# Kernel optimization log

Measured on AMD Instinct MI355X. Metric: run time of the kernel, lower is better.

## Reference

```python
import jax, jax.numpy as jnp
import numpy as np

B, S, D, H, E, TOP_K = 4, 2048, 1024, 2048, 8, 2


def setup_inputs() -> dict:
    key = jax.random.key(0)
    ks = jax.random.split(key, 5)
    scale_d = 1.0 / np.sqrt(D)
    scale_h = 1.0 / np.sqrt(H)
    return {
        "x": jax.random.normal(ks[0], (B, S, D), dtype=jnp.float32),
        "gate_w": jax.random.normal(ks[1], (D, E), dtype=jnp.float32) * scale_d,
        "w1": jax.random.normal(ks[2], (E, D, H), dtype=jnp.float32) * scale_d,
        "w2": jax.random.normal(ks[3], (E, D, H), dtype=jnp.float32) * scale_d,
        "w3": jax.random.normal(ks[4], (E, H, D), dtype=jnp.float32) * scale_h,
    }


def reference(x, gate_w, w1, w2, w3):
    # Gating: softmax over experts, keep top-k probs, renormalize.
    gate_scores = jax.nn.softmax(x @ gate_w, axis=-1)          # [B,S,E]
    top_vals, top_idx = jax.lax.top_k(gate_scores, TOP_K)      # [B,S,K]
    mask = (jax.nn.one_hot(top_idx, E, dtype=x.dtype) * top_vals[..., None]).sum(axis=-2)  # [B,S,E]
    weights = mask / (mask.sum(axis=-1, keepdims=True) + 1e-9)
    # Dense SwiGLU over ALL experts (faithful to the original ModuleList loop).
    g = jax.nn.silu(jnp.einsum('bsd,edh->bseh', x, w1)) * jnp.einsum('bsd,edh->bseh', x, w2)  # [B,S,E,H]
    expert_out = jnp.einsum('bseh,ehd->bsed', g, w3)           # [B,S,E,D]
    # Masked weighted combine (dropout is identity in eval / p=0).
    return jnp.einsum('bse,bsed->bsd', weights, expert_out)    # [B,S,D]
```

## Files before the change

kernel.cpp:

```cpp
#include <hip/hip_runtime.h>

#define T_TOK 8192
#define DDIM 1024
#define HDIM 2048
#define NEXP 8

typedef __attribute__((ext_vector_type(8))) short short8;
typedef __attribute__((ext_vector_type(4))) float f32x4;

#define WAITV8 asm volatile("s_waitcnt vmcnt(8)" ::: "memory")
#define WAITV0 asm volatile("s_waitcnt vmcnt(0)" ::: "memory")
#define WAITL0 asm volatile("s_waitcnt lgkmcnt(0)" ::: "memory")
#define SCHEDB __builtin_amdgcn_sched_barrier(0)
#define BARRIER __builtin_amdgcn_s_barrier()

__device__ __forceinline__ unsigned short f2bf(float f) {
  unsigned int u = __builtin_bit_cast(unsigned int, f);
  u += 0x7fffu + ((u >> 16) & 1u);
  return (unsigned short)(u >> 16);
}
__device__ __forceinline__ float bf2f(unsigned short h) {
  unsigned int u = ((unsigned int)h) << 16;
  return __builtin_bit_cast(float, u);
}
__device__ __forceinline__ void gload16(const void* g, void* l) {
  __builtin_amdgcn_global_load_lds((const __attribute__((address_space(1))) void*)g,
                                   (__attribute__((address_space(3))) void*)l, 16, 0, 0);
}
__device__ __forceinline__ int imin(int a, int b) { return a < b ? a : b; }

__global__ __launch_bounds__(256) void cvt_kernel(const float* __restrict__ in,
                                                  unsigned short* __restrict__ out, int n) {
  int i = (blockIdx.x * 256 + threadIdx.x) * 8;
  int stride = gridDim.x * 256 * 8;
  for (; i < n; i += stride) {
    float4 a = *(const float4*)(in + i);
    float4 b = *(const float4*)(in + i + 4);
    alignas(16) unsigned short t[8] = {f2bf(a.x), f2bf(a.y), f2bf(a.z), f2bf(a.w),
                                       f2bf(b.x), f2bf(b.y), f2bf(b.z), f2bf(b.w)};
    *(uint4*)(out + i) = *(const uint4*)t;
  }
}

__global__ __launch_bounds__(256) void tcvt_kernel(const float* __restrict__ in,
                                                   unsigned short* __restrict__ out,
                                                   int R, int C, size_t outEstride,
                                                   int perm, int s16) {
  int e = blockIdx.z;
  int rb = blockIdx.y * 64, cb = blockIdx.x * 64;
  const float* inE = in + (size_t)e * R * C;
  unsigned short* outE = out + (size_t)e * outEstride;
  __shared__ float tile[64][65];
  int tid = threadIdx.x;
  #pragma unroll
  for (int i = 0; i < 4; ++i) {
    int f = tid + i * 256;
    int r = f >> 4, c4 = (f & 15) << 2;
    float4 v = *(const float4*)(inE + (size_t)(rb + r) * C + cb + c4);
    tile[r][c4] = v.x; tile[r][c4 + 1] = v.y; tile[r][c4 + 2] = v.z; tile[r][c4 + 3] = v.w;
  }
  __syncthreads();
  #pragma unroll
  for (int i = 0; i < 2; ++i) {
    int g = tid + i * 256;
    int oc = g >> 3;
    int r8 = (g & 7) << 3;
    alignas(16) unsigned short tmp[8];
    #pragma unroll
    for (int j = 0; j < 8; ++j) tmp[j] = f2bf(tile[r8 + j][oc]);
    int orow = cb + oc;
    int orow2 = perm ? (32 * (orow >> 4) + (orow & 15) + s16) : orow;
    *(uint4*)(outE + (size_t)orow2 * R + rb + r8) = *(const uint4*)tmp;
  }
}

__global__ __launch_bounds__(256) void gate_kernel(const float* __restrict__ x,
                                                   const float* __restrict__ gw,
                                                   int* __restrict__ t_exp,
                                                   float* __restrict__ t_w) {
  int t = blockIdx.x * 4 + (threadIdx.x >> 6);
  int lane = threadIdx.x & 63;
  const float* xp = x + (size_t)t * DDIM;
  float acc[NEXP];
  #pragma unroll
  for (int e = 0; e < NEXP; ++e) acc[e] = 0.f;
  for (int i = 0; i < DDIM / 64; ++i) {
    int d = i * 64 + lane;
    float xv = xp[d];
    const float* g = gw + d * NEXP;
    #pragma unroll
    for (int e = 0; e < NEXP; ++e) acc[e] += xv * g[e];
  }
  #pragma unroll
  for (int off = 32; off > 0; off >>= 1) {
    #pragma unroll
    for (int e = 0; e < NEXP; ++e) acc[e] += __shfl_xor(acc[e], off, 64);
  }
  float mx = acc[0];
  #pragma unroll
  for (int e = 1; e < NEXP; ++e) mx = fmaxf(mx, acc[e]);
  float p[NEXP]; float S = 0.f;
  #pragma unroll
  for (int e = 0; e < NEXP; ++e) { p[e] = expf(acc[e] - mx); S += p[e]; }
  int i0 = 0; float v0 = p[0];
  #pragma unroll
  for (int e = 1; e < NEXP; ++e) if (p[e] > v0) { v0 = p[e]; i0 = e; }
  int i1 = -1; float v1 = -1.f;
  #pragma unroll
  for (int e = 0; e < NEXP; ++e) if (e != i0 && p[e] > v1) { v1 = p[e]; i1 = e; }
  float pv0 = v0 / S, pv1 = v1 / S;
  float denom = pv0 + pv1 + 1e-9f;
  if (lane == 0) {
    t_exp[t * 2] = i0; t_exp[t * 2 + 1] = i1;
    t_w[t * 2] = pv0 / denom; t_w[t * 2 + 1] = pv1 / denom;
  }
}

__global__ __launch_bounds__(1024) void partition_kernel(
    const int* __restrict__ t_exp, const float* __restrict__ t_w,
    int* __restrict__ ctrl, int* __restrict__ row_tok,
    float* __restrict__ row_w, int* __restrict__ inv_row) {
  int tid = threadIdx.x;
  int wv = tid >> 6, lane = tid & 63;
  __shared__ int wtot[16][8];
  __shared__ int wbase[16][8];
  __shared__ int soff[8];

  int t0 = tid * 8;
  int exps[16];
  int c[8];
  #pragma unroll
  for (int e = 0; e < 8; ++e) c[e] = 0;
  #pragma unroll
  for (int s = 0; s < 16; ++s) {
    exps[s] = t_exp[t0 * 2 + s];
    #pragma unroll
    for (int e = 0; e < 8; ++e) c[e] += (exps[s] == e);
  }
  int inc[8];
  #pragma unroll
  for (int e = 0; e < 8; ++e) inc[e] = c[e];
  #pragma unroll
  for (int d = 1; d < 64; d <<= 1) {
    #pragma unroll
    for (int e = 0; e < 8; ++e) {
      int v = __shfl_up(inc[e], d, 64);
      if (lane >= d) inc[e] += v;
    }
  }
  if (lane == 63) {
    #pragma unroll
    for (int e = 0; e < 8; ++e) wtot[wv][e] = inc[e];
  }
  __syncthreads();
  if (wv == 0 && lane < 16) {
    #pragma unroll
    for (int e = 0; e < 8; ++e) {
      int b = 0;
      for (int w = 0; w < 16; ++w)
        if (w < lane) b += wtot[w][e];
      wbase[lane][e] = b;
    }
  }
  __syncthreads();
  if (tid == 0) {
    int o = 0;
    #pragma unroll
    for (int e = 0; e < 8; ++e) {
      int tot = wbase[15][e] + wtot[15][e];
      ctrl[e] = tot; ctrl[8 + e] = o; soff[e] = o; o += tot;
    }
  }
  __syncthreads();
  int base[8];
  #pragma unroll
  for (int e = 0; e < 8; ++e) base[e] = soff[e] + wbase[wv][e] + (inc[e] - c[e]);
  #pragma unroll
  for (int s = 0; s < 16; ++s) {
    int ee = exps[s];
    float w = t_w[t0 * 2 + s];
    int pos = 0;
    #pragma unroll
    for (int e = 0; e < 8; ++e)
      if (ee == e) { pos = base[e]; base[e] = base[e] + 1; }
    row_tok[pos] = t0 + (s >> 1);
    row_w[pos] = w;
    inv_row[t0 * 2 + s] = pos;
  }
}


#define PHASE(B, KS, MH, STG, DOVM) do {                                   \
    short8 av[4];                                                          \
    if (MH == 0) {                                                         \
      _Pragma("unroll")                                                    \
      for (int n = 0; n < 4; ++n)                                          \
        bv[n] = *(const short8*)(&lds[B][1][KS][0] + boff + n * 512);      \
    }                                                                      \
    _Pragma("unroll")                                                      \
    for (int m = 0; m < 4; ++m)                                            \
      av[m] = *(const short8*)(&lds[B][0][KS][0] + aoff + (MH * 4 + m) * 512); \
    STG;                                                                   \
    if (DOVM) { WAITV8; }                                                  \
    BARRIER;                                                               \
    WAITL0; SCHEDB;                                                        \
    __builtin_amdgcn_s_setprio(1);                                         \
    _Pragma("unroll")                                                      \
    for (int m = 0; m < 4; ++m)                                            \
      _Pragma("unroll")                                                    \
      for (int n = 0; n < 4; ++n)                                          \
        acc[MH * 4 + m][n] = __builtin_amdgcn_mfma_f32_16x16x32_bf16(av[m], bv[n], acc[MH * 4 + m][n], 0, 0, 0); \
    __builtin_amdgcn_s_setprio(0);                                         \
    BARRIER;                                                               \
} while (0)

#define STAGE_A(B, KH, KT) do { int _o = (KT) * 64 + (KH) * 32;            \
    gload16(aSrc0 + _o, &lds[B][0][KH][0] + tid * 8);                      \
    gload16(aSrc1 + _o, &lds[B][0][KH][0] + (512 + tid) * 8); } while (0)
#define STAGE_B(B, KH, KT) do { int _o = (KT) * 64 + (KH) * 32;            \
    gload16(bSrc0 + _o, &lds[B][1][KH][0] + tid * 8);                      \
    gload16(bSrc1 + _o, &lds[B][1][KH][0] + (512 + tid) * 8); } while (0)

#define K_PIPELINE(NT)                                                     \
  WAITV0;                                                                  \
  STAGE_A(0, 0, 0); STAGE_B(0, 0, 0);                                      \
  STAGE_A(0, 1, 0); STAGE_B(0, 1, 0);                                      \
  STAGE_A(1, 0, 1); STAGE_B(1, 0, 1);                                      \
  WAITV8; BARRIER;                                                         \
  _Pragma("unroll 1")                                                      \
  for (int kt = 0; kt < (NT); kt += 2) {                                   \
    int t1 = kt + 1;                                                       \
    int t2 = imin(kt + 2, (NT) - 1), t3 = imin(kt + 3, (NT) - 1);          \
    PHASE(0, 0, 0, STAGE_A(1, 1, t1), 0);                                  \
    PHASE(0, 0, 1, STAGE_B(1, 1, t1), 1);                                  \
    PHASE(0, 1, 0, STAGE_A(0, 0, t2), 0);                                  \
    PHASE(0, 1, 1, STAGE_B(0, 0, t2), 1);                                  \
    PHASE(1, 0, 0, STAGE_A(0, 1, t2), 0);                                  \
    PHASE(1, 0, 1, STAGE_B(0, 1, t2), 1);                                  \
    PHASE(1, 1, 0, STAGE_A(1, 0, t3), 0);                                  \
    PHASE(1, 1, 1, STAGE_B(1, 0, t3), 1);                                  \
  }

__global__ __launch_bounds__(512, 1) void gemm1_kernel(
    const unsigned short* __restrict__ xbf,
    const unsigned short* __restrict__ w12t,
    const int* __restrict__ row_tok, const float* __restrict__ row_w,
    const int* __restrict__ ctrl, unsigned short* __restrict__ G) {
  int bid = blockIdx.x;
  int e = bid & 7;
  int j = bid >> 3;
  int nt = ((j >> 6) << 2) | (j & 3);
  int mt0 = (j >> 2) & 15;
  int cnt = ctrl[e];
  if (mt0 * 256 >= cnt) return;
  int off = ctrl[8 + e];

  __shared__ unsigned short lds[2][2][2][8192];

  int tid = threadIdx.x, lane = tid & 63;
  const unsigned short* w12e = w12t + (size_t)e * (4096 * 1024);

  int r0 = tid >> 2, c0 = tid & 3;
  int r1 = 128 + r0;
  int cs0 = (c0 ^ ((r0 >> 1) & 3)) * 8;
  int cs1 = (c0 ^ ((r1 >> 1) & 3)) * 8;
  const unsigned short* bSrc0 = w12e + (size_t)(nt * 256 + r0) * 1024 + cs0;
  const unsigned short* bSrc1 = w12e + (size_t)(nt * 256 + r1) * 1024 + cs1;

  int wid = tid >> 6, wr = wid >> 2, wc = wid & 3;
  int lr16 = lane & 15, hi = lane >> 4;
  int skey = (lr16 >> 1) & 3;
  int aoff = (wr * 128 + lr16) * 32 + ((hi ^ skey) * 8);
  int boff = (wc * 64 + lr16) * 32 + ((hi ^ skey) * 8);

  #pragma unroll 1
  for (int mt = mt0; mt * 256 < cnt; mt += 16) {
    int tokA = row_tok[off + imin(mt * 256 + r0, cnt - 1)];
    int tokB = row_tok[off + imin(mt * 256 + r1, cnt - 1)];
    const unsigned short* aSrc0 = xbf + (size_t)tokA * 1024 + cs0;
    const unsigned short* aSrc1 = xbf + (size_t)tokB * 1024 + cs1;

    f32x4 z = {0.f, 0.f, 0.f, 0.f};
    f32x4 acc[8][4];
    #pragma unroll
    for (int m = 0; m < 8; ++m)
      #pragma unroll
      for (int n = 0; n < 4; ++n) acc[m][n] = z;
    short8 bv[4];

    K_PIPELINE(16)

    #pragma unroll
    for (int m = 0; m < 8; ++m)
      #pragma unroll
      for (int jj = 0; jj < 4; ++jj) {
        int rl = mt * 256 + wr * 128 + m * 16 + hi * 4 + jj;
        if (rl < cnt) {
          float wrj = row_w[off + rl];
          size_t base = (size_t)(off + rl) * HDIM + nt * 128 + wc * 32 + lr16;
          float h1 = acc[m][0][jj], h2 = acc[m][1][jj];
          G[base] = f2bf((h1 / (1.f + __expf(-h1))) * h2 * wrj);
          h1 = acc[m][2][jj]; h2 = acc[m][3][jj];
          G[base + 16] = f2bf((h1 / (1.f + __expf(-h1))) * h2 * wrj);
        }
      }
  }
}

__global__ __launch_bounds__(512, 1) void gemm2_kernel(
    const unsigned short* __restrict__ G,
    const unsigned short* __restrict__ w3t,
    const int* __restrict__ ctrl, unsigned short* __restrict__ Y) {
  int bid = blockIdx.x;
  int e = bid & 7;
  int j = bid >> 3;
  int nt = j & 3;
  int mt0 = j >> 2;
  int cnt = ctrl[e];
  if (mt0 * 256 >= cnt) return;
  int off = ctrl[8 + e];

  __shared__ unsigned short lds[2][2][2][8192];

  int tid = threadIdx.x, lane = tid & 63;
  const unsigned short* w3e = w3t + (size_t)e * (1024 * 2048);

  int r0 = tid >> 2, c0 = tid & 3;
  int r1 = 128 + r0;
  int cs0 = (c0 ^ ((r0 >> 1) & 3)) * 8;
  int cs1 = (c0 ^ ((r1 >> 1) & 3)) * 8;
  const unsigned short* bSrc0 = w3e + (size_t)(nt * 256 + r0) * 2048 + cs0;
  const unsigned short* bSrc1 = w3e + (size_t)(nt * 256 + r1) * 2048 + cs1;

  int wid = tid >> 6, wr = wid >> 2, wc = wid & 3;
  int lr16 = lane & 15, hi = lane >> 4;
  int skey = (lr16 >> 1) & 3;
  int aoff = (wr * 128 + lr16) * 32 + ((hi ^ skey) * 8);
  int boff = (wc * 64 + lr16) * 32 + ((hi ^ skey) * 8);

  #pragma unroll 1
  for (int mt = mt0; mt * 256 < cnt; mt += 16) {
    const unsigned short* aSrc0 =
        G + (size_t)(off + imin(mt * 256 + r0, cnt - 1)) * 2048 + cs0;
    const unsigned short* aSrc1 =
        G + (size_t)(off + imin(mt * 256 + r1, cnt - 1)) * 2048 + cs1;

    f32x4 z = {0.f, 0.f, 0.f, 0.f};
    f32x4 acc[8][4];
    #pragma unroll
    for (int m = 0; m < 8; ++m)
      #pragma unroll
      for (int n = 0; n < 4; ++n) acc[m][n] = z;
    short8 bv[4];

    K_PIPELINE(32)

    #pragma unroll
    for (int m = 0; m < 8; ++m)
      #pragma unroll
      for (int jj = 0; jj < 4; ++jj) {
        int rl = mt * 256 + wr * 128 + m * 16 + hi * 4 + jj;
        if (rl < cnt) {
          size_t yrow = (size_t)(off + rl) * DDIM + nt * 256 + wc * 64 + lr16;
          #pragma unroll
          for (int n = 0; n < 4; ++n) Y[yrow + n * 16] = f2bf(acc[m][n][jj]);
        }
      }
  }
}

__global__ __launch_bounds__(256) void combine_kernel(const unsigned short* __restrict__ Y,
                                                      const int* __restrict__ inv_row,
                                                      float* __restrict__ out) {
  int gid = blockIdx.x * 256 + threadIdx.x;
  int t = gid >> 7;
  int cidx = (gid & 127) * 8;
  int rA = inv_row[t * 2], rB = inv_row[t * 2 + 1];
  uint4 va = *(const uint4*)(Y + (size_t)rA * DDIM + cidx);
  uint4 vb = *(const uint4*)(Y + (size_t)rB * DDIM + cidx);
  const unsigned short* pa = (const unsigned short*)&va;
  const unsigned short* pb = (const unsigned short*)&vb;
  float4 o0, o1;
  o0.x = bf2f(pa[0]) + bf2f(pb[0]); o0.y = bf2f(pa[1]) + bf2f(pb[1]);
  o0.z = bf2f(pa[2]) + bf2f(pb[2]); o0.w = bf2f(pa[3]) + bf2f(pb[3]);
  o1.x = bf2f(pa[4]) + bf2f(pb[4]); o1.y = bf2f(pa[5]) + bf2f(pb[5]);
  o1.z = bf2f(pa[6]) + bf2f(pb[6]); o1.w = bf2f(pa[7]) + bf2f(pb[7]);
  float* op = out + (size_t)t * DDIM + cidx;
  *(float4*)op = o0;
  *(float4*)(op + 4) = o1;
}

extern "C" void kernel_launch(void* const* d_in, const int* in_sizes, int n_in,
                              void* d_out, int out_size, void* d_ws, size_t ws_size,
                              hipStream_t stream) {
  const float* x  = (const float*)d_in[0];
  const float* gw = (const float*)d_in[1];
  const float* w1 = (const float*)d_in[2];
  const float* w2 = (const float*)d_in[3];
  const float* w3 = (const float*)d_in[4];
  float* out = (float*)d_out;
  char* ws = (char*)d_ws;

  unsigned short* xbf  = (unsigned short*)(ws + 0);
  unsigned short* w12t = (unsigned short*)(ws + 16777216);
  unsigned short* w3t  = (unsigned short*)(ws + 83886080);
  unsigned short* G    = (unsigned short*)(ws + 117440512);
  unsigned short* Y    = (unsigned short*)(ws + 184549376);
  int*   row_tok = (int*)  (ws + 218103808);
  float* row_w   = (float*)(ws + 218169344);
  int*   inv_row = (int*)  (ws + 218234880);
  int*   t_exp   = (int*)  (ws + 218300416);
  float* t_w     = (float*)(ws + 218365952);
  int*   ctrl    = (int*)  (ws + 218431488);

  cvt_kernel<<<4096, 256, 0, stream>>>(x, xbf, T_TOK * DDIM);
  tcvt_kernel<<<dim3(32, 16, 8), 256, 0, stream>>>(w1, w12t, 1024, 2048,
                                                   (size_t)4096 * 1024, 1, 0);
  tcvt_kernel<<<dim3(32, 16, 8), 256, 0, stream>>>(w2, w12t, 1024, 2048,
                                                   (size_t)4096 * 1024, 1, 16);
  tcvt_kernel<<<dim3(16, 32, 8), 256, 0, stream>>>(w3, w3t, 2048, 1024,
                                                   (size_t)1024 * 2048, 0, 0);

  gate_kernel<<<2048, 256, 0, stream>>>(x, gw, t_exp, t_w);
  partition_kernel<<<1, 1024, 0, stream>>>(t_exp, t_w, ctrl, row_tok, row_w, inv_row);

  gemm1_kernel<<<2048, 512, 0, stream>>>(xbf, w12t, row_tok, row_w, ctrl, G);
  gemm2_kernel<<<512, 512, 0, stream>>>(G, w3t, ctrl, Y);
  combine_kernel<<<4096, 256, 0, stream>>>(Y, inv_row, out);
}
```

Measured before the change: 393.7 us.

## Restructure MoE GEMM LDS tiles to 64-wide K with XOR swizzle and trimmed grids

Both expert GEMM kernels now stage full 64-wide K tiles per buffer, using an 8-way XOR swizzle in LDS. This replaces the previous split into two 32-wide halves. The global-to-LDS staging is reordered so each phase issues two loads and waits with vmcnt(2), and the quarter order lets the next buffer's A rows arrive just before they are read. The grids are halved, with the M-tile stride changed to 8, so fewer blocks exit early. The aim is fewer LDS bank conflicts and less wasted launch overhead, at the cost of a shallower prefetch lead that may expose memory latency.

```diff
diff --git a/kernel.cpp b/kernel.cpp
--- a/kernel.cpp
+++ b/kernel.cpp
@@ -8,7 +8,7 @@
 typedef __attribute__((ext_vector_type(8))) short short8;
 typedef __attribute__((ext_vector_type(4))) float f32x4;
 
-#define WAITV8 asm volatile("s_waitcnt vmcnt(8)" ::: "memory")
+#define WAITV2 asm volatile("s_waitcnt vmcnt(2)" ::: "memory")
 #define WAITV0 asm volatile("s_waitcnt vmcnt(0)" ::: "memory")
 #define WAITL0 asm volatile("s_waitcnt lgkmcnt(0)" ::: "memory")
 #define SCHEDB __builtin_amdgcn_sched_barrier(0)
@@ -190,18 +190,18 @@
 }
 
 
-#define PHASE(B, KS, MH, STG, DOVM) do {                                   \
+#define PHASE(B_, KS_, MH_, STG) do {                                      \
     short8 av[4];                                                          \
-    if (MH == 0) {                                                         \
+    if (MH_ == 0) {                                                        \
       _Pragma("unroll")                                                    \
       for (int n = 0; n < 4; ++n)                                          \
-        bv[n] = *(const short8*)(&lds[B][1][KS][0] + boff + n * 512);      \
+        bv[n] = *(const short8*)(&lds[B_][1][0] + bR + cK[KS_] + n * 1024);\
     }                                                                      \
     _Pragma("unroll")                                                      \
     for (int m = 0; m < 4; ++m)                                            \
-      av[m] = *(const short8*)(&lds[B][0][KS][0] + aoff + (MH * 4 + m) * 512); \
+      av[m] = *(const short8*)(&lds[B_][0][0] + aR + cK[KS_] + (MH_ * 4 + m) * 1024); \
     STG;                                                                   \
-    if (DOVM) { WAITV8; }                                                  \
+    WAITV2;                                                                \
     BARRIER;                                                               \
     WAITL0; SCHEDB;                                                        \
     __builtin_amdgcn_s_setprio(1);                                         \
@@ -209,36 +209,28 @@
     for (int m = 0; m < 4; ++m)                                            \
       _Pragma("unroll")                                                    \
       for (int n = 0; n < 4; ++n)                                          \
-        acc[MH * 4 + m][n] = __builtin_amdgcn_mfma_f32_16x16x32_bf16(av[m], bv[n], acc[MH * 4 + m][n], 0, 0, 0); \
+        acc[MH_ * 4 + m][n] = __builtin_amdgcn_mfma_f32_16x16x32_bf16(av[m], bv[n], acc[MH_ * 4 + m][n], 0, 0, 0); \
     __builtin_amdgcn_s_setprio(0);                                         \
     BARRIER;                                                               \
 } while (0)
 
-#define STAGE_A(B, KH, KT) do { int _o = (KT) * 64 + (KH) * 32;            \
-    gload16(aSrc0 + _o, &lds[B][0][KH][0] + tid * 8);                      \
-    gload16(aSrc1 + _o, &lds[B][0][KH][0] + (512 + tid) * 8); } while (0)
-#define STAGE_B(B, KH, KT) do { int _o = (KT) * 64 + (KH) * 32;            \
-    gload16(bSrc0 + _o, &lds[B][1][KH][0] + tid * 8);                      \
-    gload16(bSrc1 + _o, &lds[B][1][KH][0] + (512 + tid) * 8); } while (0)
-
 #define K_PIPELINE(NT)                                                     \
   WAITV0;                                                                  \
-  STAGE_A(0, 0, 0); STAGE_B(0, 0, 0);                                      \
-  STAGE_A(0, 1, 0); STAGE_B(0, 1, 0);                                      \
-  STAGE_A(1, 0, 1); STAGE_B(1, 0, 1);                                      \
-  WAITV8; BARRIER;                                                         \
+  STB(0, 0, 0); STB(0, 1, 0); STB(0, 2, 0); STB(0, 3, 0);                  \
+  STA(0, 0, 0); STA(0, 1, 0); STA(0, 2, 0); STA(0, 3, 0);                  \
+  WAITV0; BARRIER;                                                         \
   _Pragma("unroll 1")                                                      \
   for (int kt = 0; kt < (NT); kt += 2) {                                   \
     int t1 = kt + 1;                                                       \
-    int t2 = imin(kt + 2, (NT) - 1), t3 = imin(kt + 3, (NT) - 1);          \
-    PHASE(0, 0, 0, STAGE_A(1, 1, t1), 0);                                  \
-    PHASE(0, 0, 1, STAGE_B(1, 1, t1), 1);                                  \
-    PHASE(0, 1, 0, STAGE_A(0, 0, t2), 0);                                  \
-    PHASE(0, 1, 1, STAGE_B(0, 0, t2), 1);                                  \
-    PHASE(1, 0, 0, STAGE_A(0, 1, t2), 0);                                  \
-    PHASE(1, 0, 1, STAGE_B(0, 1, t2), 1);                                  \
-    PHASE(1, 1, 0, STAGE_A(1, 0, t3), 0);                                  \
-    PHASE(1, 1, 1, STAGE_B(1, 0, t3), 1);                                  \
+    int t2 = imin(kt + 2, (NT) - 1);                                       \
+    PHASE(0, 0, 0, { STB(1, 0, t1); STB(1, 1, t1); });                     \
+    PHASE(0, 0, 1, { STB(1, 2, t1); STB(1, 3, t1); });                     \
+    PHASE(0, 1, 0, { STA(1, 0, t1); STA(1, 2, t1); });                     \
+    PHASE(0, 1, 1, { STA(1, 1, t1); STA(1, 3, t1); });                     \
+    PHASE(1, 0, 0, { STB(0, 0, t2); STB(0, 1, t2); });                     \
+    PHASE(1, 0, 1, { STB(0, 2, t2); STB(0, 3, t2); });                     \
+    PHASE(1, 1, 0, { STA(0, 0, t2); STA(0, 2, t2); });                     \
+    PHASE(1, 1, 1, { STA(0, 1, t2); STA(0, 3, t2); });                     \
   }
 
 __global__ __launch_bounds__(512, 1) void gemm1_kernel(
@@ -249,37 +241,38 @@
   int bid = blockIdx.x;
   int e = bid & 7;
   int j = bid >> 3;
-  int nt = ((j >> 6) << 2) | (j & 3);
-  int mt0 = (j >> 2) & 15;
+  int nt = ((j >> 5) << 2) | (j & 3);
+  int mt0 = (j >> 2) & 7;
   int cnt = ctrl[e];
   if (mt0 * 256 >= cnt) return;
   int off = ctrl[8 + e];
 
-  __shared__ unsigned short lds[2][2][2][8192];
+  __shared__ unsigned short lds[2][2][16384];
 
   int tid = threadIdx.x, lane = tid & 63;
   const unsigned short* w12e = w12t + (size_t)e * (4096 * 1024);
 
-  int r0 = tid >> 2, c0 = tid & 3;
-  int r1 = 128 + r0;
-  int cs0 = (c0 ^ ((r0 >> 1) & 3)) * 8;
-  int cs1 = (c0 ^ ((r1 >> 1) & 3)) * 8;
-  const unsigned short* bSrc0 = w12e + (size_t)(nt * 256 + r0) * 1024 + cs0;
-  const unsigned short* bSrc1 = w12e + (size_t)(nt * 256 + r1) * 1024 + cs1;
+  int sr = tid >> 3;
+  int cS8 = ((tid & 7) ^ (sr & 7)) * 8;
+  const unsigned short* bQ = w12e + (size_t)(nt * 256 + sr) * 1024 + cS8;
 
   int wid = tid >> 6, wr = wid >> 2, wc = wid & 3;
   int lr16 = lane & 15, hi = lane >> 4;
-  int skey = (lr16 >> 1) & 3;
-  int aoff = (wr * 128 + lr16) * 32 + ((hi ^ skey) * 8);
-  int boff = (wc * 64 + lr16) * 32 + ((hi ^ skey) * 8);
+  int cK[2] = { ((hi) ^ (lr16 & 7)) * 8, ((4 | hi) ^ (lr16 & 7)) * 8 };
+  int aR = (wr * 128 + lr16) * 64;
+  int bR = (wc * 64 + lr16) * 64;
+
+#define STA(B_, Q_, KT) gload16(aQ[Q_] + (KT) * 64, &lds[B_][0][0] + (Q_) * 4096 + tid * 8)
+#define STB(B_, Q_, KT) gload16(bQ + (Q_) * 65536 + (KT) * 64, &lds[B_][1][0] + (Q_) * 4096 + tid * 8)
 
   #pragma unroll 1
-  for (int mt = mt0; mt * 256 < cnt; mt += 16) {
-    int tokA = row_tok[off + imin(mt * 256 + r0, cnt - 1)];
-    int tokB = row_tok[off + imin(mt * 256 + r1, cnt - 1)];
-    const unsigned short* aSrc0 = xbf + (size_t)tokA * 1024 + cs0;
-    const unsigned short* aSrc1 = xbf + (size_t)tokB * 1024 + cs1;
-
+  for (int mt = mt0; mt * 256 < cnt; mt += 8) {
+    const unsigned short* aQ[4];
+    #pragma unroll
+    for (int q = 0; q < 4; ++q) {
+      int tok = row_tok[off + imin(mt * 256 + q * 64 + sr, cnt - 1)];
+      aQ[q] = xbf + (size_t)tok * 1024 + cS8;
+    }
     f32x4 z = {0.f, 0.f, 0.f, 0.f};
     f32x4 acc[8][4];
     #pragma unroll
@@ -294,7 +287,8 @@
     for (int m = 0; m < 8; ++m)
       #pragma unroll
       for (int jj = 0; jj < 4; ++jj) {
-        int rl = mt * 256 + wr * 128 + m * 16 + hi * 4 + jj;
+        int rl = mt * 256 + ((m >> 2) ? (64 + wr * 128) : (wr * 128)) + (m & 3) * 16 + hi * 4 + jj;
+        rl = mt * 256 + wr * 128 + (m >> 2) * 64 + (m & 3) * 16 + hi * 4 + jj;
         if (rl < cnt) {
           float wrj = row_w[off + rl];
           size_t base = (size_t)(off + rl) * HDIM + nt * 128 + wc * 32 + lr16;
@@ -305,6 +299,8 @@
         }
       }
   }
+#undef STA
+#undef STB
 }
 
 __global__ __launch_bounds__(512, 1) void gemm2_kernel(
@@ -314,36 +310,36 @@
   int bid = blockIdx.x;
   int e = bid & 7;
   int j = bid >> 3;
-  int nt = j & 3;
-  int mt0 = j >> 2;
+  int nt = j >> 3;
+  int mt0 = j & 7;
   int cnt = ctrl[e];
   if (mt0 * 256 >= cnt) return;
   int off = ctrl[8 + e];
 
-  __shared__ unsigned short lds[2][2][2][8192];
+  __shared__ unsigned short lds[2][2][16384];
 
   int tid = threadIdx.x, lane = tid & 63;
   const unsigned short* w3e = w3t + (size_t)e * (1024 * 2048);
 
-  int r0 = tid >> 2, c0 = tid & 3;
-  int r1 = 128 + r0;
-  int cs0 = (c0 ^ ((r0 >> 1) & 3)) * 8;
-  int cs1 = (c0 ^ ((r1 >> 1) & 3)) * 8;
-  const unsigned short* bSrc0 = w3e + (size_t)(nt * 256 + r0) * 2048 + cs0;
-  const unsigned short* bSrc1 = w3e + (size_t)(nt * 256 + r1) * 2048 + cs1;
+  int sr = tid >> 3;
+  int cS8 = ((tid & 7) ^ (sr & 7)) * 8;
+  const unsigned short* bQ = w3e + (size_t)(nt * 256 + sr) * 2048 + cS8;
 
   int wid = tid >> 6, wr = wid >> 2, wc = wid & 3;
   int lr16 = lane & 15, hi = lane >> 4;
-  int skey = (lr16 >> 1) & 3;
-  int aoff = (wr * 128 + lr16) * 32 + ((hi ^ skey) * 8);
-  int boff = (wc * 64 + lr16) * 32 + ((hi ^ skey) * 8);
+  int cK[2] = { ((hi) ^ (lr16 & 7)) * 8, ((4 | hi) ^ (lr16 & 7)) * 8 };
+  int aR = (wr * 128 + lr16) * 64;
+  int bR = (wc * 64 + lr16) * 64;
+
+#define STA(B_, Q_, KT) gload16(aQ[Q_] + (KT) * 64, &lds[B_][0][0] + (Q_) * 4096 + tid * 8)
+#define STB(B_, Q_, KT) gload16(bQ + (Q_) * 131072 + (KT) * 64, &lds[B_][1][0] + (Q_) * 4096 + tid * 8)
 
   #pragma unroll 1
-  for (int mt = mt0; mt * 256 < cnt; mt += 16) {
-    const unsigned short* aSrc0 =
-        G + (size_t)(off + imin(mt * 256 + r0, cnt - 1)) * 2048 + cs0;
-    const unsigned short* aSrc1 =
-        G + (size_t)(off + imin(mt * 256 + r1, cnt - 1)) * 2048 + cs1;
+  for (int mt = mt0; mt * 256 < cnt; mt += 8) {
+    const unsigned short* aQ[4];
+    #pragma unroll
+    for (int q = 0; q < 4; ++q)
+      aQ[q] = G + (size_t)(off + imin(mt * 256 + q * 64 + sr, cnt - 1)) * 2048 + cS8;
 
     f32x4 z = {0.f, 0.f, 0.f, 0.f};
     f32x4 acc[8][4];
@@ -359,7 +355,7 @@
     for (int m = 0; m < 8; ++m)
       #pragma unroll
       for (int jj = 0; jj < 4; ++jj) {
-        int rl = mt * 256 + wr * 128 + m * 16 + hi * 4 + jj;
+        int rl = mt * 256 + wr * 128 + (m >> 2) * 64 + (m & 3) * 16 + hi * 4 + jj;
         if (rl < cnt) {
           size_t yrow = (size_t)(off + rl) * DDIM + nt * 256 + wc * 64 + lr16;
           #pragma unroll
@@ -367,6 +363,8 @@
         }
       }
   }
+#undef STA
+#undef STB
 }
 
 __global__ __launch_bounds__(256) void combine_kernel(const unsigned short* __restrict__ Y,
@@ -424,7 +422,7 @@
   gate_kernel<<<2048, 256, 0, stream>>>(x, gw, t_exp, t_w);
   partition_kernel<<<1, 1024, 0, stream>>>(t_exp, t_w, ctrl, row_tok, row_w, inv_row);
 
-  gemm1_kernel<<<2048, 512, 0, stream>>>(xbf, w12t, row_tok, row_w, ctrl, G);
-  gemm2_kernel<<<512, 512, 0, stream>>>(G, w3t, ctrl, Y);
+  gemm1_kernel<<<1024, 512, 0, stream>>>(xbf, w12t, row_tok, row_w, ctrl, G);
+  gemm2_kernel<<<256, 512, 0, stream>>>(G, w3t, ctrl, Y);
   combine_kernel<<<4096, 256, 0, stream>>>(Y, inv_row, out);
 }
```

Measured after the change: 390.6 us. About the same (-0.8%).
